# Performance work log

Measured on AMD Instinct MI355X. Metric: run time of the kernel, lower is better.

## Reference

```python
import jax, jax.numpy as jnp
import numpy as np

EMB_DIM = 32
UID_TGT = 200000
IID_TGT = 50000
BATCH = 128
TOPK = 50000          # hardcoded inside test_source_free branch
TARGET_LABEL = 4.0    # module-level target rating constant


def setup_inputs() -> dict:
    key = jax.random.key(0)
    k1, k2, k3, k4, k5 = jax.random.split(key, 5)
    # x: column 0 = item id (stored as float, like the torch code), cols 1: = src_rate_pre
    iid = jax.random.randint(k1, (BATCH,), 0, IID_TGT).astype(jnp.float32)
    src_rate = jax.random.normal(k2, (BATCH, EMB_DIM), dtype=jnp.float32)
    x = jnp.concatenate([iid[:, None], src_rate], axis=1)  # [B, 1+D]
    uid_weight = 0.1 * jax.random.normal(k3, (UID_TGT, EMB_DIM), dtype=jnp.float32)
    iid_weight = 0.1 * jax.random.normal(k4, (IID_TGT, EMB_DIM), dtype=jnp.float32)
    rp_weight = 0.1 * jax.random.normal(k5, (EMB_DIM, EMB_DIM), dtype=jnp.float32)
    return {"x": x, "uid_weight": uid_weight, "iid_weight": iid_weight, "rp_weight": rp_weight}


def reference(x, uid_weight, iid_weight, rp_weight):
    # === stage == 'test_source_free' ===
    iid = x[:, 0].astype(jnp.int32)                     # [B]
    iid_emb = iid_weight[iid]                           # [B, D] item embedding gather
    src_rate_pre = x[:, 1:] @ rp_weight.T               # [B, D] Linear(emb,emb,bias=False)
    # |uid_emb . src_rate - target|  (torch: [U,B]; here kept [B,U])
    predict_rate = jnp.abs(src_rate_pre @ uid_weight.T - TARGET_LABEL)  # [B, U]
    # torch: full sort ascending + take first TOPK  ==  bottom-TOPK per row
    _, topk_idx = jax.lax.top_k(-predict_rate, TOPK)    # [B, TOPK]
    # voted rating = <selected user emb, item emb>; compute all dots once,
    # then gather (same math as gathering [B,TOPK,D] embeddings and dotting).
    all_scores = iid_emb @ uid_weight.T                 # [B, U]
    voted_rating = jnp.take_along_axis(all_scores, topk_idx, axis=1)  # [B, TOPK]
    mean_rating = jnp.mean(voted_rating, axis=1)        # [B]
    return mean_rating
```

## Files before the change

kernel.cpp:

```cpp
#include <hip/hip_runtime.h>
#include <hip/hip_bf16.h>
#include <stdint.h>

#define EMB    32
#define BATCH  128
#define NU     200000
#define KSEL   50000
#define XCOLS  33
#define SLOTS  64

#define OFF_SPRE   0
#define OFF_IIDE   16384
#define OFF_GHIST  32768
#define OFF_BASE16 163840
#define OFF_PREFIX 164352
#define OFF_M2     164864
#define OFF_EQ     165376
#define OFF_CAND   173568

__global__ void prep_kernel(const float* __restrict__ x,
                            const float* __restrict__ iid_w,
                            const float* __restrict__ rp,
                            const float* __restrict__ uid,
                            float* __restrict__ s_pre,
                            float* __restrict__ iid_emb,
                            uint32_t* __restrict__ base16) {
    const int b = blockIdx.x;
    const int t = threadIdx.x;
    __shared__ float xr[EMB];
    if (t < EMB) xr[t] = x[b * XCOLS + 1 + t];
    __syncthreads();
    if (t < EMB) {
        float acc = 0.f;
        #pragma unroll
        for (int k = 0; k < EMB; ++k) acc += xr[k] * rp[t * EMB + k];
        s_pre[b * EMB + t] = acc;
    } else {
        const int d = t - EMB;
        const int iid = (int)x[b * XCOLS];
        iid_emb[b * EMB + d] = iid_w[(size_t)iid * EMB + d];
    }
    __syncthreads();
    if (t == 0) {
        float dot = 0.f;
        #pragma unroll
        for (int k = 0; k < EMB; ++k) dot += s_pre[b * EMB + k] * uid[k];
        const uint32_t bits = __float_as_uint(fabsf(dot - 4.0f));
        const uint32_t hi = bits >> 16;
        base16[b] = (hi > 128u) ? (hi - 128u) : 0u;
    }
}

__global__ void zero_kernel(uint32_t* __restrict__ p, int n) {
    int i = blockIdx.x * blockDim.x + threadIdx.x;
    if (i < n) p[i] = 0u;
}

__global__ __launch_bounds__(1024)
void sweep1_kernel(const float* __restrict__ s_pre,
                   const float* __restrict__ uid,
                   const uint32_t* __restrict__ base16,
                   uint32_t* __restrict__ ghist,
                   int jchunk) {
    extern __shared__ uint32_t hist[];
    const int t  = threadIdx.x;
    const int b  = t & 127;
    const int jl = t >> 7;
    for (int i = t; i < 128 * 257; i += 1024) hist[i] = 0u;
    float s[EMB];
    #pragma unroll
    for (int d = 0; d < EMB; ++d) s[d] = s_pre[b * EMB + d];
    const uint32_t base = base16[b];
    __syncthreads();

    const int j0 = blockIdx.x * jchunk;
    const int jend = min(j0 + jchunk, NU);
    int j = j0 + jl;
    for (; j + 8 < jend; j += 16) {
        const int ju = __builtin_amdgcn_readfirstlane(j);
        const float* up0 = uid + (size_t)ju * EMB;
        const float* up1 = up0 + 8 * EMB;
        float d0 = 0.f, d1 = 0.f;
        #pragma unroll
        for (int k = 0; k < EMB; ++k) {
            d0 += s[k] * up0[k];
            d1 += s[k] * up1[k];
        }
        const uint32_t bits0 = __float_as_uint(fabsf(d0 - 4.0f));
        const uint32_t bits1 = __float_as_uint(fabsf(d1 - 4.0f));
        int dg0 = (int)(bits0 >> 16) - (int)base; dg0 = dg0 < 0 ? 0 : (dg0 > 255 ? 255 : dg0);
        int dg1 = (int)(bits1 >> 16) - (int)base; dg1 = dg1 < 0 ? 0 : (dg1 > 255 ? 255 : dg1);
        atomicAdd(&hist[b * 257 + dg0], 1u);
        atomicAdd(&hist[b * 257 + dg1], 1u);
    }
    for (; j < jend; j += 8) {
        const int ju = __builtin_amdgcn_readfirstlane(j);
        const float* up0 = uid + (size_t)ju * EMB;
        float d0 = 0.f;
        #pragma unroll
        for (int k = 0; k < EMB; ++k) d0 += s[k] * up0[k];
        const uint32_t bits0 = __float_as_uint(fabsf(d0 - 4.0f));
        int dg0 = (int)(bits0 >> 16) - (int)base; dg0 = dg0 < 0 ? 0 : (dg0 > 255 ? 255 : dg0);
        atomicAdd(&hist[b * 257 + dg0], 1u);
    }
    __syncthreads();
    for (int i = t; i < 128 * 256; i += 1024) {
        const uint32_t c = hist[(i >> 8) * 257 + (i & 255)];
        if (c) atomicAdd(&ghist[i], c);
    }
}

__global__ void scan1_kernel(const uint32_t* __restrict__ ghist,
                             const uint32_t* __restrict__ base16,
                             uint32_t* __restrict__ prefix16,
                             uint32_t* __restrict__ m2) {
    const int b = threadIdx.x;
    uint32_t cum = 0, before = 0;
    int c1 = 255;
    for (int d = 0; d < 256; ++d) {
        const uint32_t c = ghist[b * 256 + d];
        if (cum + c >= (uint32_t)KSEL) { c1 = d; before = cum; break; }
        cum += c;
        if (d == 255) before = cum;
    }
    prefix16[b] = base16[b] + (uint32_t)c1;
    m2[b] = (uint32_t)KSEL - before;
}

__global__ __launch_bounds__(1024)
void sweep2_kernel(const float* __restrict__ s_pre,
                   const float* __restrict__ iid_emb,
                   const float* __restrict__ uid,
                   const uint32_t* __restrict__ prefix16,
                   uint32_t* __restrict__ eq_cnt,
                   float* __restrict__ sum_part,
                   uint64_t* __restrict__ cand,
                   int cap, int jchunk) {
    extern __shared__ char smem2[];
    uint64_t* lcand = (uint64_t*)smem2;
    uint32_t* lcnt  = (uint32_t*)(smem2 + 65536);
    uint32_t* lbase = (uint32_t*)(smem2 + 66048);
    float*    sums  = (float*)(smem2 + 66560);
    const int t  = threadIdx.x;
    const int b  = t & 127;
    const int jl = t >> 7;
    if (t < 128) lcnt[t] = 0u;
    float s[EMB], e[EMB];
    #pragma unroll
    for (int d = 0; d < EMB; ++d) { s[d] = s_pre[b*EMB+d]; e[d] = iid_emb[b*EMB+d]; }
    const uint32_t pfx = prefix16[b];
    __syncthreads();

    const int j0 = blockIdx.x * jchunk;
    const int jend = min(j0 + jchunk, NU);
    float local = 0.f;
    int j = j0 + jl;
    for (; j + 8 < jend; j += 16) {
        const int ju = __builtin_amdgcn_readfirstlane(j);
        const float* up0 = uid + (size_t)ju * EMB;
        const float* up1 = up0 + 8 * EMB;
        float d0 = 0.f, v0 = 0.f, d1 = 0.f, v1 = 0.f;
        #pragma unroll
        for (int k = 0; k < EMB; ++k) {
            const float u0 = up0[k], u1 = up1[k];
            d0 += s[k] * u0;  v0 += e[k] * u0;
            d1 += s[k] * u1;  v1 += e[k] * u1;
        }
        const uint32_t bits0 = __float_as_uint(fabsf(d0 - 4.0f));
        const uint32_t bits1 = __float_as_uint(fabsf(d1 - 4.0f));
        const uint32_t hi0 = bits0 >> 16, hi1 = bits1 >> 16;
        if (hi0 < pfx) local += v0;
        else if (hi0 == pfx) {
            const uint32_t pos = atomicAdd(&lcnt[b], 1u);
            const uint64_t pk = ((uint64_t)bits0 << 32) | (uint32_t)j;
            if (pos < (uint32_t)SLOTS) lcand[b * SLOTS + pos] = pk;
            else {
                const uint32_t g = atomicAdd(&eq_cnt[b * 16], 1u);
                if (g < (uint32_t)cap) cand[(size_t)b * cap + g] = pk;
            }
        }
        if (hi1 < pfx) local += v1;
        else if (hi1 == pfx) {
            const uint32_t pos = atomicAdd(&lcnt[b], 1u);
            const uint64_t pk = ((uint64_t)bits1 << 32) | (uint32_t)(j + 8);
            if (pos < (uint32_t)SLOTS) lcand[b * SLOTS + pos] = pk;
            else {
                const uint32_t g = atomicAdd(&eq_cnt[b * 16], 1u);
                if (g < (uint32_t)cap) cand[(size_t)b * cap + g] = pk;
            }
        }
    }
    for (; j < jend; j += 8) {
        const int ju = __builtin_amdgcn_readfirstlane(j);
        const float* up0 = uid + (size_t)ju * EMB;
        float d0 = 0.f, v0 = 0.f;
        #pragma unroll
        for (int k = 0; k < EMB; ++k) {
            const float u0 = up0[k];
            d0 += s[k] * u0;  v0 += e[k] * u0;
        }
        const uint32_t bits0 = __float_as_uint(fabsf(d0 - 4.0f));
        const uint32_t hi0 = bits0 >> 16;
        if (hi0 < pfx) local += v0;
        else if (hi0 == pfx) {
            const uint32_t pos = atomicAdd(&lcnt[b], 1u);
            const uint64_t pk = ((uint64_t)bits0 << 32) | (uint32_t)j;
            if (pos < (uint32_t)SLOTS) lcand[b * SLOTS + pos] = pk;
            else {
                const uint32_t g = atomicAdd(&eq_cnt[b * 16], 1u);
                if (g < (uint32_t)cap) cand[(size_t)b * cap + g] = pk;
            }
        }
    }
    sums[t] = local;
    __syncthreads();
    if (t < 128) {
        float acc = 0.f;
        #pragma unroll
        for (int l = 0; l < 8; ++l) acc += sums[l * 128 + t];
        sum_part[blockIdx.x * 128 + t] = acc;
        const uint32_t n = min(lcnt[t], (uint32_t)SLOTS);
        lbase[t] = atomicAdd(&eq_cnt[t * 16], n);
    }
    __syncthreads();
    for (int i = t; i < 128 * SLOTS; i += 1024) {
        const int bb = i >> 6;
        const int sl = i & 63;
        if (sl < (int)min(lcnt[bb], (uint32_t)SLOTS)) {
            const uint32_t p = lbase[bb] + (uint32_t)sl;
            if (p < (uint32_t)cap) cand[(size_t)bb * cap + p] = lcand[i];
        }
    }
}

__global__ __launch_bounds__(256)
void final_kernel(const float* __restrict__ iid_emb,
                  const float* __restrict__ uid,
                  const uint32_t* __restrict__ m2_,
                  const uint32_t* __restrict__ eq_cnt,
                  const float* __restrict__ sum_part,
                  const uint64_t* __restrict__ cand,
                  int cap, float* __restrict__ out) {
    const int b = blockIdx.x;
    const int t = threadIdx.x;
    __shared__ float red[256];
    __shared__ uint32_t hist[256];
    __shared__ float e[EMB];
    __shared__ uint32_t tie[128];
    __shared__ uint32_t tiecnt, sc2, sm3, sc3, sm4;
    __shared__ float sbelow;
    if (t < EMB) e[t] = iid_emb[b * EMB + t];
    if (t == 0) tiecnt = 0u;
    hist[t] = 0u;
    red[t] = sum_part[t * 128 + b];
    __syncthreads();
    for (int s = 128; s > 0; s >>= 1) { if (t < s) red[t] += red[t + s]; __syncthreads(); }
    if (t == 0) sbelow = red[0];
    __syncthreads();

    const uint32_t ec = eq_cnt[b * 16];
    const int cnt = (int)(ec < (uint32_t)cap ? ec : (uint32_t)cap);
    const uint64_t* cb = cand + (size_t)b * cap;

    for (int i = t; i < cnt; i += 256) {
        const uint32_t low16 = (uint32_t)(cb[i] >> 32) & 0xFFFFu;
        atomicAdd(&hist[low16 >> 8], 1u);
    }
    __syncthreads();
    if (t == 0) {
        const uint32_t m2v = m2_[b];
        uint32_t cum = 0, before = 0; int c2 = 255;
        for (int d = 0; d < 256; ++d) {
            const uint32_t c = hist[d];
            if (cum + c >= m2v) { c2 = d; before = cum; break; }
            cum += c;
        }
        sc2 = (uint32_t)c2; sm3 = m2v - before;
    }
    __syncthreads();
    const uint32_t c2 = sc2;
    hist[t] = 0u;
    __syncthreads();

    for (int i = t; i < cnt; i += 256) {
        const uint32_t low16 = (uint32_t)(cb[i] >> 32) & 0xFFFFu;
        if ((low16 >> 8) == c2) atomicAdd(&hist[low16 & 255u], 1u);
    }
    __syncthreads();
    if (t == 0) {
        const uint32_t m3 = sm3;
        uint32_t cum = 0, before = 0; int c3 = 255;
        for (int d = 0; d < 256; ++d) {
            const uint32_t c = hist[d];
            if (cum + c >= m3) { c3 = d; before = cum; break; }
            cum += c;
        }
        sc3 = (uint32_t)c3; sm4 = m3 - before;
    }
    __syncthreads();
    const uint32_t T16 = (c2 << 8) | sc3;

    float local = 0.f;
    for (int i = t; i < cnt; i += 256) {
        const uint64_t cv = cb[i];
        const uint32_t low16 = (uint32_t)(cv >> 32) & 0xFFFFu;
        if (low16 < T16) {
            const uint32_t j = (uint32_t)cv;
            const float4* u4 = (const float4*)(uid + (size_t)j * EMB);
            float dv = 0.f;
            #pragma unroll
            for (int q = 0; q < 8; ++q) {
                float4 u = u4[q];
                dv += e[4*q+0]*u.x + e[4*q+1]*u.y + e[4*q+2]*u.z + e[4*q+3]*u.w;
            }
            local += dv;
        } else if (low16 == T16) {
            const uint32_t pos = atomicAdd(&tiecnt, 1u);
            if (pos < 128u) tie[pos] = (uint32_t)cv;
        }
    }
    red[t] = local;
    __syncthreads();
    for (int s = 128; s > 0; s >>= 1) { if (t < s) red[t] += red[t + s]; __syncthreads(); }
    if (t == 0) {
        int tc = (int)(tiecnt < 128u ? tiecnt : 128u);
        for (int i = 1; i < tc; ++i) {
            const uint32_t v = tie[i]; int k = i - 1;
            while (k >= 0 && tie[k] > v) { tie[k+1] = tie[k]; --k; }
            tie[k+1] = v;
        }
        const int m4 = (int)sm4;
        float tsum = 0.f;
        for (int i = 0; i < m4 && i < tc; ++i) {
            const uint32_t j = tie[i];
            float dv = 0.f;
            for (int d = 0; d < EMB; ++d) dv += e[d] * uid[(size_t)j * EMB + d];
            tsum += dv;
        }
        out[b] = (sbelow + red[0] + tsum) / (float)KSEL;
    }
}

extern "C" void kernel_launch(void* const* d_in, const int* in_sizes, int n_in,
                              void* d_out, int out_size, void* d_ws, size_t ws_size,
                              hipStream_t stream) {
    const float* x     = (const float*)d_in[0];
    const float* uid   = (const float*)d_in[1];
    const float* iid_w = (const float*)d_in[2];
    const float* rp    = (const float*)d_in[3];
    float* out = (float*)d_out;

    char* ws = (char*)d_ws;
    float*    s_pre    = (float*)(ws + OFF_SPRE);
    float*    iid_emb  = (float*)(ws + OFF_IIDE);
    uint32_t* ghist    = (uint32_t*)(ws + OFF_GHIST);
    float*    sum_part = (float*)(ws + OFF_GHIST);
    uint32_t* base16   = (uint32_t*)(ws + OFF_BASE16);
    uint32_t* prefix16 = (uint32_t*)(ws + OFF_PREFIX);
    uint32_t* m2       = (uint32_t*)(ws + OFF_M2);
    uint32_t* eq_cnt   = (uint32_t*)(ws + OFF_EQ);
    uint64_t* cand     = (uint64_t*)(ws + OFF_CAND);

    long long cap_ll = ((long long)ws_size - OFF_CAND) / (128LL * 8LL);
    int cap = (int)(cap_ll > 16384 ? 16384 : (cap_ll < 1 ? 1 : cap_ll));

    {
        const int n = (OFF_CAND - OFF_GHIST) / 4;
        zero_kernel<<<(n + 255) / 256, 256, 0, stream>>>((uint32_t*)(ws + OFF_GHIST), n);
    }
    prep_kernel<<<BATCH, 64, 0, stream>>>(x, iid_w, rp, uid, s_pre, iid_emb, base16);

    const int JC = 782;
    const int G  = 256;
    sweep1_kernel<<<G, 1024, 128 * 257 * 4, stream>>>(s_pre, uid, base16, ghist, JC);

    scan1_kernel<<<1, 128, 0, stream>>>(ghist, base16, prefix16, m2);

    sweep2_kernel<<<G, 1024, 65536 + 512 + 512 + 4096, stream>>>(s_pre, iid_emb, uid,
                                                                 prefix16, eq_cnt, sum_part,
                                                                 cand, cap, JC);

    final_kernel<<<BATCH, 256, 0, stream>>>(iid_emb, uid, m2, eq_cnt, sum_part,
                                            cand, cap, out);
}
```

Baseline: 210.9 us.

## Replace global histogram atomics with per-block partials and parallel scan

Sweep1 now writes each block's full 128x256 histogram to a per-block partial buffer with vector stores instead of issuing global atomics. A new scan kernel with one block per batch row reduces the partials in parallel, replacing the single-block serial scan. Launch bounds gain a min-blocks hint, and the sweep2 below-threshold accumulation becomes branch-free. This needs 32MB of extra workspace and falls back to the old path when the workspace is too small. The reduction kernel reads that whole buffer, trading atomic contention for memory traffic.

```diff
diff --git a/kernel.cpp b/kernel.cpp
--- a/kernel.cpp
+++ b/kernel.cpp
@@ -8,6 +8,7 @@
 #define KSEL   50000
 #define XCOLS  33
 #define SLOTS  64
+#define NBLK   256
 
 #define OFF_SPRE   0
 #define OFF_IIDE   16384
@@ -17,6 +18,8 @@
 #define OFF_M2     164864
 #define OFF_EQ     165376
 #define OFF_CAND   173568
+#define OFF_PART   173568
+#define PART_BYTES ((size_t)NBLK * 128 * 256 * 4)
 
 __global__ void prep_kernel(const float* __restrict__ x,
                             const float* __restrict__ iid_w,
@@ -56,11 +59,12 @@
     if (i < n) p[i] = 0u;
 }
 
-__global__ __launch_bounds__(1024)
+template <bool PART>
+__global__ __launch_bounds__(1024, 4)
 void sweep1_kernel(const float* __restrict__ s_pre,
                    const float* __restrict__ uid,
                    const uint32_t* __restrict__ base16,
-                   uint32_t* __restrict__ ghist,
+                   uint32_t* __restrict__ gout,
                    int jchunk) {
     extern __shared__ uint32_t hist[];
     const int t  = threadIdx.x;
@@ -104,9 +108,22 @@
         atomicAdd(&hist[b * 257 + dg0], 1u);
     }
     __syncthreads();
-    for (int i = t; i < 128 * 256; i += 1024) {
-        const uint32_t c = hist[(i >> 8) * 257 + (i & 255)];
-        if (c) atomicAdd(&ghist[i], c);
+    if (PART) {
+        uint32_t* part = gout + (size_t)blockIdx.x * 32768;
+        for (int i = t * 4; i < 32768; i += 4096) {
+            const int row = i >> 8, d = i & 255;
+            uint4 v;
+            v.x = hist[row * 257 + d + 0];
+            v.y = hist[row * 257 + d + 1];
+            v.z = hist[row * 257 + d + 2];
+            v.w = hist[row * 257 + d + 3];
+            *(uint4*)(part + i) = v;
+        }
+    } else {
+        for (int i = t; i < 128 * 256; i += 1024) {
+            const uint32_t c = hist[(i >> 8) * 257 + (i & 255)];
+            if (c) atomicAdd(&gout[i], c);
+        }
     }
 }
 
@@ -127,7 +144,38 @@
     m2[b] = (uint32_t)KSEL - before;
 }
 
-__global__ __launch_bounds__(1024)
+__global__ __launch_bounds__(256)
+void scan1_part_kernel(const uint32_t* __restrict__ part,
+                       const uint32_t* __restrict__ base16,
+                       uint32_t* __restrict__ prefix16,
+                       uint32_t* __restrict__ m2) {
+    const int row = blockIdx.x;
+    const int t = threadIdx.x;
+    __shared__ uint32_t h[256];
+    uint32_t a0 = 0, a1 = 0, a2 = 0, a3 = 0;
+    const uint32_t* p = part + (size_t)row * 256 + t;
+    for (int g = 0; g < NBLK; g += 4) {
+        a0 += p[(size_t)(g + 0) * 32768];
+        a1 += p[(size_t)(g + 1) * 32768];
+        a2 += p[(size_t)(g + 2) * 32768];
+        a3 += p[(size_t)(g + 3) * 32768];
+    }
+    h[t] = a0 + a1 + a2 + a3;
+    __syncthreads();
+    if (t == 0) {
+        uint32_t cum = 0, before = 0; int c1 = 255;
+        for (int d = 0; d < 256; ++d) {
+            const uint32_t c = h[d];
+            if (cum + c >= (uint32_t)KSEL) { c1 = d; before = cum; break; }
+            cum += c;
+            if (d == 255) before = cum;
+        }
+        prefix16[row] = base16[row] + (uint32_t)c1;
+        m2[row] = (uint32_t)KSEL - before;
+    }
+}
+
+__global__ __launch_bounds__(1024, 4)
 void sweep2_kernel(const float* __restrict__ s_pre,
                    const float* __restrict__ iid_emb,
                    const float* __restrict__ uid,
@@ -169,8 +217,9 @@
         const uint32_t bits0 = __float_as_uint(fabsf(d0 - 4.0f));
         const uint32_t bits1 = __float_as_uint(fabsf(d1 - 4.0f));
         const uint32_t hi0 = bits0 >> 16, hi1 = bits1 >> 16;
-        if (hi0 < pfx) local += v0;
-        else if (hi0 == pfx) {
+        local += (hi0 < pfx) ? v0 : 0.f;
+        local += (hi1 < pfx) ? v1 : 0.f;
+        if (hi0 == pfx) {
             const uint32_t pos = atomicAdd(&lcnt[b], 1u);
             const uint64_t pk = ((uint64_t)bits0 << 32) | (uint32_t)j;
             if (pos < (uint32_t)SLOTS) lcand[b * SLOTS + pos] = pk;
@@ -179,8 +228,7 @@
                 if (g < (uint32_t)cap) cand[(size_t)b * cap + g] = pk;
             }
         }
-        if (hi1 < pfx) local += v1;
-        else if (hi1 == pfx) {
+        if (hi1 == pfx) {
             const uint32_t pos = atomicAdd(&lcnt[b], 1u);
             const uint64_t pk = ((uint64_t)bits1 << 32) | (uint32_t)(j + 8);
             if (pos < (uint32_t)SLOTS) lcand[b * SLOTS + pos] = pk;
@@ -201,8 +249,8 @@
         }
         const uint32_t bits0 = __float_as_uint(fabsf(d0 - 4.0f));
         const uint32_t hi0 = bits0 >> 16;
-        if (hi0 < pfx) local += v0;
-        else if (hi0 == pfx) {
+        local += (hi0 < pfx) ? v0 : 0.f;
+        if (hi0 == pfx) {
             const uint32_t pos = atomicAdd(&lcnt[b], 1u);
             const uint64_t pk = ((uint64_t)bits0 << 32) | (uint32_t)j;
             if (pos < (uint32_t)SLOTS) lcand[b * SLOTS + pos] = pk;
@@ -359,10 +407,22 @@
     uint32_t* prefix16 = (uint32_t*)(ws + OFF_PREFIX);
     uint32_t* m2       = (uint32_t*)(ws + OFF_M2);
     uint32_t* eq_cnt   = (uint32_t*)(ws + OFF_EQ);
-    uint64_t* cand     = (uint64_t*)(ws + OFF_CAND);
-
-    long long cap_ll = ((long long)ws_size - OFF_CAND) / (128LL * 8LL);
-    int cap = (int)(cap_ll > 16384 ? 16384 : (cap_ll < 1 ? 1 : cap_ll));
+    uint32_t* part     = (uint32_t*)(ws + OFF_PART);
+
+    const size_t off_cand2 = OFF_PART + PART_BYTES;
+    const bool use_part = ws_size >= off_cand2 + (size_t)128 * 8 * 4096;
+
+    uint64_t* cand;
+    int cap;
+    if (use_part) {
+        cand = (uint64_t*)(ws + off_cand2);
+        long long cap_ll = ((long long)ws_size - (long long)off_cand2) / (128LL * 8LL);
+        cap = (int)(cap_ll > 16384 ? 16384 : cap_ll);
+    } else {
+        cand = (uint64_t*)(ws + OFF_CAND);
+        long long cap_ll = ((long long)ws_size - OFF_CAND) / (128LL * 8LL);
+        cap = (int)(cap_ll > 16384 ? 16384 : (cap_ll < 1 ? 1 : cap_ll));
+    }
 
     {
         const int n = (OFF_CAND - OFF_GHIST) / 4;
@@ -371,14 +431,17 @@
     prep_kernel<<<BATCH, 64, 0, stream>>>(x, iid_w, rp, uid, s_pre, iid_emb, base16);
 
     const int JC = 782;
-    const int G  = 256;
-    sweep1_kernel<<<G, 1024, 128 * 257 * 4, stream>>>(s_pre, uid, base16, ghist, JC);
-
-    scan1_kernel<<<1, 128, 0, stream>>>(ghist, base16, prefix16, m2);
-
-    sweep2_kernel<<<G, 1024, 65536 + 512 + 512 + 4096, stream>>>(s_pre, iid_emb, uid,
-                                                                 prefix16, eq_cnt, sum_part,
-                                                                 cand, cap, JC);
+    if (use_part) {
+        sweep1_kernel<true><<<NBLK, 1024, 128 * 257 * 4, stream>>>(s_pre, uid, base16, part, JC);
+        scan1_part_kernel<<<BATCH, 256, 0, stream>>>(part, base16, prefix16, m2);
+    } else {
+        sweep1_kernel<false><<<NBLK, 1024, 128 * 257 * 4, stream>>>(s_pre, uid, base16, ghist, JC);
+        scan1_kernel<<<1, 128, 0, stream>>>(ghist, base16, prefix16, m2);
+    }
+
+    sweep2_kernel<<<NBLK, 1024, 65536 + 512 + 512 + 4096, stream>>>(s_pre, iid_emb, uid,
+                                                                    prefix16, eq_cnt, sum_part,
+                                                                    cand, cap, JC);
 
     final_kernel<<<BATCH, 256, 0, stream>>>(iid_emb, uid, m2, eq_cnt, sum_part,
                                             cand, cap, out);
```

Measured after the change: 238.7 us. 13.2% more time.
